# Performance work log

Measured on AMD Instinct MI355X. Metric: run time of the kernel, lower is better.

Reference implementation:

```python
import jax, jax.numpy as jnp
import numpy as np

WL, FL = 64, 40
SCALE = 2.0 ** FL
CLIP_MAX = 2.0 ** (WL - FL - 1) - 2.0 ** (-FL)  # (2^(wl-1)-1)/2^fl
CLIP_MIN = -(2.0 ** (WL - FL - 1))
EPS = 1e-5
H = 8  # num_heads


def quant(x):
    # Fixed-point nearest-rounding quantizer: wl=64, fl=40.
    return jnp.clip(jnp.round(x * SCALE) / SCALE, CLIP_MIN, CLIP_MAX)


def setup_inputs() -> dict:
    key = jax.random.key(0)
    ks = jax.random.split(key, 9)
    N, S, C = 4096, 31, 512  # S = num_particles + 1 = 31 (hard-coded in module)
    SS = S * S
    return {
        "x": jax.random.normal(ks[0], (N, S, C), dtype=jnp.float32),
        "norm_gamma": jnp.ones((C,), jnp.float32),
        "norm_beta": jnp.zeros((C,), jnp.float32),
        "wq": jax.random.normal(ks[1], (C, C), jnp.float32) * 0.02,
        "wk": jax.random.normal(ks[2], (C, C), jnp.float32) * 0.02,
        "wv": jax.random.normal(ks[3], (C, C), jnp.float32) * 0.02,
        "wo": jax.random.normal(ks[4], (C, C), jnp.float32) * 0.02,
        "bo": jnp.zeros((C,), jnp.float32),
        "pre_gamma": jnp.ones((SS,), jnp.float32),
        "pre_beta": jnp.zeros((SS,), jnp.float32),
    }


def reference(x, norm_gamma, norm_beta, wq, wk, wv, wo, bo, pre_gamma, pre_beta):
    N, S, C = x.shape
    # BatchNorm1d(C) on x.transpose(1,2): per-channel stats over (batch, seq), training-mode (batch stats)
    mu = jnp.mean(x, axis=(0, 1))
    var = jnp.var(x, axis=(0, 1))
    out = quant((x - mu) * jax.lax.rsqrt(var + EPS) * norm_gamma + norm_beta)

    out_q = quant(out @ wq.T)
    out_k = quant(out @ wk.T)
    out_v = quant(out @ wv.T)

    q_ = out_q.reshape(N, S, H, C // H)
    k_ = out_k.reshape(N, S, H, C // H)
    v_ = out_v.reshape(N, S, H, C // H)

    energy = quant(jnp.einsum('nqhc,nkhc->nhqk', q_, k_))  # [N,H,S,S]

    # pre_exp_norm: BatchNorm1d(S*S) over reshaped energies; channel dim = S*S, stats over (batch, heads)
    e = energy.reshape(N, H, S * S)
    em = jnp.mean(e, axis=(0, 1))
    ev = jnp.var(e, axis=(0, 1))
    en = quant((e - em) * jax.lax.rsqrt(ev + EPS) * pre_gamma + pre_beta)
    energy_post = en.reshape(N, H, S, S)

    attention = quant(jax.nn.softmax(energy_post / jnp.sqrt(jnp.float32(C)), axis=-1))

    out = quant(jnp.einsum('nhql,nlhc->nqhc', attention, v_)).reshape(N, S, C)
    out = quant(out @ wo.T + bo)
    return quant(out + x)
```

## Files before the change

### kernel.cpp

```cpp
#include <hip/hip_runtime.h>
#include <cstdint>
#include <cstddef>

#define N_ 4096
#define S_ 31
#define C_ 512
#define H_ 8
#define M_ (N_*S_)
#define NH_ (N_*H_)

typedef unsigned short u16;
typedef unsigned char  u8;
typedef __bf16 v8bf __attribute__((ext_vector_type(8)));
typedef float  v4f  __attribute__((ext_vector_type(4)));
typedef float  v2f  __attribute__((ext_vector_type(2)));
typedef unsigned short v8u __attribute__((ext_vector_type(8)));
typedef unsigned short v4u __attribute__((ext_vector_type(4)));

#define WS_STATS 2097152
#define WS_Q (WS_STATS + 32768)
#define WS_K (WS_Q + 67108864)
#define WS_V (WS_K + 67108864)

#define SCALE_QK 16.0f
#define SCALE_V  16.0f

__device__ __forceinline__ u16 f2bf(float f) {
  union { float f; unsigned u; } v; v.f = f;
  unsigned r = v.u + 0x7FFFu + ((v.u >> 16) & 1u);
  return (u16)(r >> 16);
}
__device__ __forceinline__ float bf2f(u16 v) {
  union { unsigned u; float f; } w; w.u = ((unsigned)v) << 16; return w.f;
}
__device__ __forceinline__ unsigned enc4(float a, float b, float c, float d) {
  int w = __builtin_amdgcn_cvt_pk_fp8_f32(a, b, 0, false);
  w = __builtin_amdgcn_cvt_pk_fp8_f32(c, d, w, true);
  return (unsigned)w;
}
__device__ __forceinline__ v8bf dec8(uint2 u) {
  v2f p0 = __builtin_amdgcn_cvt_pk_f32_fp8((int)u.x, false);
  v2f p1 = __builtin_amdgcn_cvt_pk_f32_fp8((int)u.x, true);
  v2f p2 = __builtin_amdgcn_cvt_pk_f32_fp8((int)u.y, false);
  v2f p3 = __builtin_amdgcn_cvt_pk_f32_fp8((int)u.y, true);
  v8bf r;
  r[0]=(__bf16)p0[0]; r[1]=(__bf16)p0[1]; r[2]=(__bf16)p1[0]; r[3]=(__bf16)p1[1];
  r[4]=(__bf16)p2[0]; r[5]=(__bf16)p2[1]; r[6]=(__bf16)p3[0]; r[7]=(__bf16)p3[1];
  return r;
}

__global__ void k_init(const float* wq, const float* wk, const float* wv, const float* wo,
                       u16* wbf, float* statsf) {
  int gid = blockIdx.x * 256 + threadIdx.x;
  if (gid < 6144) statsf[gid] = 0.0f;
  int m = gid >> 18, o = gid & 262143;
  int e    = o & 7;
  int lane = (o >> 3) & 63;
  int kk   = (o >> 9) & 15;
  int j16  = o >> 13;
  int j = j16 * 16 + (lane & 15);
  int k = kk * 32 + (lane >> 4) * 8 + e;
  const float* src = (m == 0) ? wq : (m == 1) ? wk : (m == 2) ? wv : wo;
  wbf[(size_t)m * 262144 + o] = f2bf(src[j * 512 + k]);
}

__global__ void __launch_bounds__(512, 8) k_xstats(const float* __restrict__ x, float* statsf) {
  __shared__ float4 rs[512], rq[512];
  int t = threadIdx.x;
  int c4 = (t & 127) * 4;
  int r0 = blockIdx.x * 128 + (t >> 7) * 32;
  float4 s = {0,0,0,0}, sq = {0,0,0,0};
  const float* p = x + (size_t)r0 * C_ + c4;
  for (int i = 0; i < 32; ++i) {
    float4 v = *(const float4*)(p + (size_t)i * C_);
    s.x += v.x; s.y += v.y; s.z += v.z; s.w += v.w;
    sq.x += v.x*v.x; sq.y += v.y*v.y; sq.z += v.z*v.z; sq.w += v.w*v.w;
  }
  rs[t] = s; rq[t] = sq;
  __syncthreads();
  if (t < 128) {
    #pragma unroll
    for (int g = 1; g < 4; ++g) {
      float4 a = rs[t + g*128], b = rq[t + g*128];
      s.x += a.x; s.y += a.y; s.z += a.z; s.w += a.w;
      sq.x += b.x; sq.y += b.y; sq.z += b.z; sq.w += b.w;
    }
    atomicAdd(&statsf[c4+0], s.x); atomicAdd(&statsf[c4+1], s.y);
    atomicAdd(&statsf[c4+2], s.z); atomicAdd(&statsf[c4+3], s.w);
    atomicAdd(&statsf[512+c4+0], sq.x); atomicAdd(&statsf[512+c4+1], sq.y);
    atomicAdd(&statsf[512+c4+2], sq.z); atomicAdd(&statsf[512+c4+3], sq.w);
  }
}

__device__ __forceinline__ void gemm64(const u16* sa, const u16* B0, v4f (&acc)[4][4], int lane) {
  #pragma unroll
  for (int m = 0; m < 4; ++m)
    #pragma unroll
    for (int c = 0; c < 4; ++c) acc[m][c] = (v4f){0,0,0,0};
  #pragma unroll 2
  for (int kk = 0; kk < 16; ++kk) {
    v8bf a[4], b[4];
    #pragma unroll
    for (int m = 0; m < 4; ++m)
      a[m] = *(const v8bf*)(sa + ((((kk*4 + m) << 6) | (lane ^ (kk & 7))) << 3));
    #pragma unroll
    for (int c = 0; c < 4; ++c)
      b[c] = *(const v8bf*)(B0 + (size_t)c * 8192 + kk * 512);
    #pragma unroll
    for (int m = 0; m < 4; ++m)
      #pragma unroll
      for (int c = 0; c < 4; ++c)
        acc[m][c] = __builtin_amdgcn_mfma_f32_16x16x32_bf16(a[m], b[c], acc[m][c], 0, 0, 0);
  }
}

__global__ void __launch_bounds__(512, 4)
k_qkv(const float* __restrict__ x, const u16* __restrict__ wbf,
      const float* __restrict__ statsf, const float* __restrict__ gamma,
      const float* __restrict__ beta, u8* __restrict__ eg8, u8* __restrict__ vt) {
  __shared__ float s_scale[C_], s_shift[C_];
  __shared__ u16 s_a[16*4*64*8];
  int t = threadIdx.x, nblk = blockIdx.x;
  int wave = t >> 6, lane = t & 63, l15 = lane & 15, quad = lane >> 4;
  {
    float su = statsf[t], sqv = statsf[512 + t];
    float mu  = su * (1.0f / (float)M_);
    float var = sqv * (1.0f / (float)M_) - mu * mu;
    float sc  = rsqrtf(var + 1e-5f) * gamma[t];
    s_scale[t] = sc;
    s_shift[t] = beta[t] - mu * sc;
  }
  __syncthreads();

  const float* xb = x + (size_t)nblk * 2 * S_ * C_;
  for (int it = 0; it < 8; ++it) {
    int idx = t + it * 512;
    int row = idx >> 6, c8 = (idx & 63) << 3;
    int nl = row >> 5, s = row & 31;
    int kk = c8 >> 5, q4 = (c8 >> 3) & 3, mt = row >> 4, r15 = row & 15;
    u16* dst = s_a + ((((kk*4 + mt) << 6) | ((q4*16 + r15) ^ (kk & 7))) << 3);
    v8u o;
    if (s == 31) { o = (v8u){0,0,0,0,0,0,0,0}; }
    else {
      const float* g = xb + (size_t)(nl * 31 + s) * C_ + c8;
      float4 a = *(const float4*)g, b = *(const float4*)(g + 4);
      o[0]=f2bf(a.x*s_scale[c8+0]+s_shift[c8+0]); o[1]=f2bf(a.y*s_scale[c8+1]+s_shift[c8+1]);
      o[2]=f2bf(a.z*s_scale[c8+2]+s_shift[c8+2]); o[3]=f2bf(a.w*s_scale[c8+3]+s_shift[c8+3]);
      o[4]=f2bf(b.x*s_scale[c8+4]+s_shift[c8+4]); o[5]=f2bf(b.y*s_scale[c8+5]+s_shift[c8+5]);
      o[6]=f2bf(b.z*s_scale[c8+6]+s_shift[c8+6]); o[7]=f2bf(b.w*s_scale[c8+7]+s_shift[c8+7]);
    }
    *(v8u*)dst = o;
  }
  __syncthreads();

  v4f acc[4][4];

  gemm64(s_a, wbf + (size_t)2 * 262144 + (size_t)wave * 32768 + (size_t)lane * 8, acc, lane);
  #pragma unroll
  for (int m = 0; m < 4; ++m) {
    int rbase = m*16 + quad*4;
    int nl = rbase >> 5, s0 = rbase & 31;
    size_t nbase = (size_t)(nblk*2 + nl) * 8;
    #pragma unroll
    for (int c = 0; c < 4; ++c) {
      int d = c*16 + l15;
      unsigned w = enc4(acc[m][c][0]*SCALE_V, acc[m][c][1]*SCALE_V,
                        acc[m][c][2]*SCALE_V, acc[m][c][3]*SCALE_V);
      *(unsigned*)(vt + ((nbase + wave) * 2048) + d*32 + s0) = w;
    }
  }

  unsigned qpack[16];
  gemm64(s_a, wbf + (size_t)0 * 262144 + (size_t)wave * 32768 + (size_t)lane * 8, acc, lane);
  #pragma unroll
  for (int m = 0; m < 4; ++m)
    #pragma unroll
    for (int c = 0; c < 4; ++c)
      qpack[m*4+c] = enc4(acc[m][c][0]*SCALE_QK, acc[m][c][1]*SCALE_QK,
                          acc[m][c][2]*SCALE_QK, acc[m][c][3]*SCALE_QK);

  unsigned kpack[16];
  gemm64(s_a, wbf + (size_t)1 * 262144 + (size_t)wave * 32768 + (size_t)lane * 8, acc, lane);
  #pragma unroll
  for (int m = 0; m < 4; ++m)
    #pragma unroll
    for (int c = 0; c < 4; ++c)
      kpack[m*4+c] = enc4(acc[m][c][0]*SCALE_QK, acc[m][c][1]*SCALE_QK,
                          acc[m][c][2]*SCALE_QK, acc[m][c][3]*SCALE_QK);

  __syncthreads();

  u8* scr = (u8*)s_a + wave * 8192;
  #pragma unroll
  for (int m = 0; m < 4; ++m)
    #pragma unroll
    for (int c = 0; c < 4; ++c) {
      int d = c*16 + l15;
      #pragma unroll
      for (int reg = 0; reg < 4; ++reg) {
        int r = m*16 + quad*4 + reg;
        int dd = d ^ ((r & 7) << 3);
        scr[r*64 + dd]        = (u8)(qpack[m*4+c] >> (reg*8));
        scr[4096 + r*64 + dd] = (u8)(kpack[m*4+c] >> (reg*8));
      }
    }

  const float inv = 1.0f / (SCALE_QK * SCALE_QK);
  #pragma unroll 1
  for (int n = 0; n < 2; ++n) {
    v8bf A[2][2], B[2][2];
    #pragma unroll
    for (int mt = 0; mt < 2; ++mt)
      #pragma unroll
      for (int kk = 0; kk < 2; ++kk) {
        int r = n*32 + mt*16 + l15;
        int dA = (kk*32 + quad*8) ^ ((r & 7) << 3);
        A[mt][kk] = dec8(*(const uint2*)(scr + r*64 + dA));
        B[mt][kk] = dec8(*(const uint2*)(scr + 4096 + r*64 + dA));
      }
    u16* ep = (u16*)(eg8 + (((size_t)(nblk*2 + n) * 8 + wave) * 2048));
    #pragma unroll
    for (int qt = 0; qt < 2; ++qt)
      #pragma unroll
      for (int kt = 0; kt < 2; ++kt) {
        v4f a2 = {0,0,0,0};
        a2 = __builtin_amdgcn_mfma_f32_16x16x32_bf16(A[qt][0], B[kt][0], a2, 0, 0, 0);
        a2 = __builtin_amdgcn_mfma_f32_16x16x32_bf16(A[qt][1], B[kt][1], a2, 0, 0, 0);
        int k = kt*16 + l15;
        #pragma unroll
        for (int reg = 0; reg < 4; ++reg) {
          int q = qt*16 + quad*4 + reg;
          ep[q*32 + k] = f2bf(a2[reg] * inv);
        }
      }
  }
}

__global__ void __launch_bounds__(256, 8) k_estats(const u16* __restrict__ eg, float* statsf) {
  int t = threadIdx.x;
  int r0 = blockIdx.x * 32;
  float s[4] = {0,0,0,0}, sq[4] = {0,0,0,0};
  for (int i = 0; i < 32; ++i) {
    uint2 u = *(const uint2*)(eg + (size_t)(r0 + i) * 1024 + t * 4);
    float v0 = bf2f((u16)(u.x & 0xffff)), v1 = bf2f((u16)(u.x >> 16));
    float v2 = bf2f((u16)(u.y & 0xffff)), v3 = bf2f((u16)(u.y >> 16));
    s[0]+=v0; s[1]+=v1; s[2]+=v2; s[3]+=v3;
    sq[0]+=v0*v0; sq[1]+=v1*v1; sq[2]+=v2*v2; sq[3]+=v3*v3;
  }
  #pragma unroll
  for (int j = 0; j < 4; ++j) {
    atomicAdd(&statsf[2048 + t*4 + j], s[j]);
    atomicAdd(&statsf[3072 + t*4 + j], sq[j]);
  }
}

__global__ void k_finalize_e(const float* pg, const float* pb, float* statsf) {
  int c = threadIdx.x;
  int q = c >> 5, k = c & 31;
  const float invC = 0.04419417382415922f;
  float s2 = 0.f, sh2 = 0.f;
  if (q < 31 && k < 31) {
    int ss = q*31 + k;
    float mu  = statsf[2048 + c] * (1.0f / (float)NH_);
    float var = statsf[3072 + c] * (1.0f / (float)NH_) - mu * mu;
    float sc  = rsqrtf(var + 1e-5f) * pg[ss];
    s2  = sc * invC;
    sh2 = (pb[ss] - mu * sc) * invC;
  }
  statsf[4096 + c] = s2;
  statsf[5120 + c] = sh2;
}

__global__ void __launch_bounds__(512, 4)
k_oproj(const float* __restrict__ x, const u16* __restrict__ wbf,
        const float* __restrict__ statsf, const u16* __restrict__ eg,
        const u8* __restrict__ vt, const float* __restrict__ bo, float* __restrict__ out) {
  __shared__ u16 s_a[16*4*64*8];
  __shared__ u16 s_attn[8][1024];
  int t = threadIdx.x, nblk = blockIdx.x;
  int wave = t >> 6, lane = t & 63, l15 = lane & 15, quad = lane >> 4;

  int q = lane & 31, half = lane >> 5;
  #pragma unroll 1
  for (int tk = 0; tk < 2; ++tk) {
    int task = wave * 2 + tk;
    int nl = task >> 3, h = task & 7;
    size_t nh = (size_t)(nblk*2 + nl) * 8 + h;
    const u16* ep = eg + nh * 1024;
    int cb = q*32 + half*16;
    v8u e0 = *(const v8u*)(ep + cb);
    v8u e1 = *(const v8u*)(ep + cb + 8);
    const float* s2g  = statsf + 4096 + cb;
    const float* sh2g = statsf + 5120 + cb;
    float lg[16];
    #pragma unroll
    for (int j = 0; j < 8; ++j) lg[j]   = bf2f(e0[j]) * s2g[j]   + sh2g[j];
    #pragma unroll
    for (int j = 0; j < 8; ++j) lg[8+j] = bf2f(e1[j]) * s2g[8+j] + sh2g[8+j];
    if (half) lg[15] = -1e30f;
    float mx = lg[0];
    #pragma unroll
    for (int j = 1; j < 16; ++j) mx = fmaxf(mx, lg[j]);
    mx = fmaxf(mx, __shfl_xor(mx, 32));
    float sum = 0.f;
    #pragma unroll
    for (int j = 0; j < 16; ++j) { lg[j] = __expf(lg[j] - mx); sum += lg[j]; }
    sum += __shfl_xor(sum, 32);
    float r = (q == 31) ? 0.f : (1.0f / sum);
    v8u o0, o1;
    #pragma unroll
    for (int j = 0; j < 8; ++j) { o0[j] = f2bf(lg[j] * r); o1[j] = f2bf(lg[8+j] * r); }
    *(v8u*)(&s_attn[wave][cb]) = o0;
    *(v8u*)(&s_attn[wave][cb + 8]) = o1;
    v8bf a0 = *(const v8bf*)(&s_attn[wave][(l15)*32 + quad*8]);
    v8bf a1 = *(const v8bf*)(&s_attn[wave][(16 + l15)*32 + quad*8]);
    const float invV = 1.0f / SCALE_V;
    #pragma unroll
    for (int ct = 0; ct < 4; ++ct) {
      uint2 u = *(const uint2*)(vt + nh*2048 + (ct*16 + l15)*32 + quad*8);
      v8bf b = dec8(u);
      v4f c0 = {0,0,0,0}, c1 = {0,0,0,0};
      c0 = __builtin_amdgcn_mfma_f32_16x16x32_bf16(b, a0, c0, 0, 0, 0);
      c1 = __builtin_amdgcn_mfma_f32_16x16x32_bf16(b, a1, c1, 0, 0, 0);
      int kkA = h*2 + (ct>>1);
      int qA  = (ct*2 + (quad>>1)) & 3;
      int pA  = (quad&1)*4;
      v4u w0, w1;
      #pragma unroll
      for (int reg = 0; reg < 4; ++reg) {
        w0[reg] = f2bf(c0[reg] * invV);
        w1[reg] = f2bf(c1[reg] * invV);
      }
      *(v4u*)(&s_a[((((kkA*4 + nl*2 + 0) << 6) | (qA*16 + l15)) << 3) + pA]) = w0;
      *(v4u*)(&s_a[((((kkA*4 + nl*2 + 1) << 6) | (qA*16 + l15)) << 3) + pA]) = w1;
    }
  }
  __syncthreads();

  {
    const u16* B0 = wbf + (size_t)3 * 262144 + (size_t)wave * 32768 + (size_t)lane * 8;
    v4f acc[4][4];
    #pragma unroll
    for (int m = 0; m < 4; ++m)
      #pragma unroll
      for (int c = 0; c < 4; ++c) acc[m][c] = (v4f){0,0,0,0};
    #pragma unroll 2
    for (int kk = 0; kk < 16; ++kk) {
      v8bf a[4], b[4];
      #pragma unroll
      for (int m = 0; m < 4; ++m)
        a[m] = *(const v8bf*)(s_a + ((((kk*4 + m) << 6) | lane) << 3));
      #pragma unroll
      for (int c = 0; c < 4; ++c)
        b[c] = *(const v8bf*)(B0 + (size_t)c * 8192 + kk * 512);
      #pragma unroll
      for (int m = 0; m < 4; ++m)
        #pragma unroll
        for (int c = 0; c < 4; ++c)
          acc[m][c] = __builtin_amdgcn_mfma_f32_16x16x32_bf16(a[m], b[c], acc[m][c], 0, 0, 0);
    }
    #pragma unroll
    for (int m = 0; m < 4; ++m) {
      int rbase = m*16 + quad*4;
      int nl = rbase >> 5, s0 = rbase & 31;
      #pragma unroll
      for (int c = 0; c < 4; ++c) {
        int j = wave*64 + c*16 + l15;
        float bj = bo[j];
        #pragma unroll
        for (int reg = 0; reg < 4; ++reg) {
          int s = s0 + reg;
          if (s < 31) {
            size_t off = (size_t)((nblk*2 + nl) * 31 + s) * C_ + j;
            out[off] = acc[m][c][reg] + bj + x[off];
          }
        }
      }
    }
  }
}

extern "C" void kernel_launch(void* const* d_in, const int* in_sizes, int n_in,
                              void* d_out, int out_size, void* d_ws, size_t ws_size,
                              hipStream_t stream) {
  const float* x     = (const float*)d_in[0];
  const float* gamma = (const float*)d_in[1];
  const float* beta  = (const float*)d_in[2];
  const float* wq    = (const float*)d_in[3];
  const float* wk    = (const float*)d_in[4];
  const float* wv    = (const float*)d_in[5];
  const float* wo    = (const float*)d_in[6];
  const float* bo    = (const float*)d_in[7];
  const float* pg    = (const float*)d_in[8];
  const float* pb    = (const float*)d_in[9];

  char* ws = (char*)d_ws;
  u16*   wbf    = (u16*)ws;
  float* statsf = (float*)(ws + WS_STATS);
  u8*    eg8    = (u8*)(ws + WS_Q);
  u8*    vtp    = (u8*)(ws + WS_V);
  float* outp   = (float*)d_out;

  k_init<<<4096, 256, 0, stream>>>(wq, wk, wv, wo, wbf, statsf);
  k_xstats<<<992, 512, 0, stream>>>(x, statsf);
  k_qkv<<<2048, 512, 0, stream>>>(x, wbf, statsf, gamma, beta, eg8, vtp);
  k_estats<<<1024, 256, 0, stream>>>((const u16*)eg8, statsf);
  k_finalize_e<<<1, 1024, 0, stream>>>(pg, pb, statsf);
  k_oproj<<<2048, 512, 0, stream>>>(x, wbf, statsf, (const u16*)eg8, vtp, bo, outp);
}
```

Measured before the change: 1.009 ms.

## Split GEMM tiles into 64x32 halves with register-prefetched weight fragments

Each wave's 64x64 GEMM tile is now computed as two 64x32 halves, so it holds 8 accumulators instead of 16. A three-slot rotating buffer prefetches the global weight fragments two k-steps ahead, hiding global load latency behind the MFMAs. The intent is to cut register pressure to fit the launch bound of 4 blocks per CU and to overlap weight loads with compute. In exchange, the LDS A fragments are read twice per tile, and the fully unrolled loop grows code size.

```diff
diff --git a/kernel.cpp b/kernel.cpp
--- a/kernel.cpp
+++ b/kernel.cpp
@@ -92,25 +92,34 @@
   }
 }
 
-__device__ __forceinline__ void gemm64(const u16* sa, const u16* B0, v4f (&acc)[4][4], int lane) {
+template<int SWZ>
+__device__ __forceinline__ void gemm64x32(const u16* sa, const u16* B0, v4f (&acc)[4][2], int lane) {
   #pragma unroll
   for (int m = 0; m < 4; ++m)
     #pragma unroll
-    for (int c = 0; c < 4; ++c) acc[m][c] = (v4f){0,0,0,0};
-  #pragma unroll 2
+    for (int c = 0; c < 2; ++c) acc[m][c] = (v4f){0,0,0,0};
+  v8bf b[3][2];
+  #pragma unroll
+  for (int p = 0; p < 2; ++p)
+    #pragma unroll
+    for (int c = 0; c < 2; ++c)
+      b[p][c] = *(const v8bf*)(B0 + (size_t)c * 8192 + p * 512);
+  #pragma unroll
   for (int kk = 0; kk < 16; ++kk) {
-    v8bf a[4], b[4];
+    if (kk + 2 < 16) {
+      #pragma unroll
+      for (int c = 0; c < 2; ++c)
+        b[(kk+2)%3][c] = *(const v8bf*)(B0 + (size_t)c * 8192 + (kk+2) * 512);
+    }
+    v8bf a[4];
     #pragma unroll
     for (int m = 0; m < 4; ++m)
-      a[m] = *(const v8bf*)(sa + ((((kk*4 + m) << 6) | (lane ^ (kk & 7))) << 3));
-    #pragma unroll
-    for (int c = 0; c < 4; ++c)
-      b[c] = *(const v8bf*)(B0 + (size_t)c * 8192 + kk * 512);
+      a[m] = *(const v8bf*)(sa + ((((kk*4 + m) << 6) | (SWZ ? (lane ^ (kk & 7)) : lane)) << 3));
     #pragma unroll
     for (int m = 0; m < 4; ++m)
       #pragma unroll
-      for (int c = 0; c < 4; ++c)
-        acc[m][c] = __builtin_amdgcn_mfma_f32_16x16x32_bf16(a[m], b[c], acc[m][c], 0, 0, 0);
+      for (int c = 0; c < 2; ++c)
+        acc[m][c] = __builtin_amdgcn_mfma_f32_16x16x32_bf16(a[m], b[kk%3][c], acc[m][c], 0, 0, 0);
   }
 }
 
@@ -153,40 +162,50 @@
   }
   __syncthreads();
 
-  v4f acc[4][4];
-
-  gemm64(s_a, wbf + (size_t)2 * 262144 + (size_t)wave * 32768 + (size_t)lane * 8, acc, lane);
-  #pragma unroll
-  for (int m = 0; m < 4; ++m) {
-    int rbase = m*16 + quad*4;
-    int nl = rbase >> 5, s0 = rbase & 31;
-    size_t nbase = (size_t)(nblk*2 + nl) * 8;
-    #pragma unroll
-    for (int c = 0; c < 4; ++c) {
-      int d = c*16 + l15;
-      unsigned w = enc4(acc[m][c][0]*SCALE_V, acc[m][c][1]*SCALE_V,
-                        acc[m][c][2]*SCALE_V, acc[m][c][3]*SCALE_V);
-      *(unsigned*)(vt + ((nbase + wave) * 2048) + d*32 + s0) = w;
+  #pragma unroll
+  for (int cs = 0; cs < 2; ++cs) {
+    v4f acc[4][2];
+    gemm64x32<1>(s_a, wbf + (size_t)2 * 262144 + (size_t)wave * 32768 + cs * 16384 + (size_t)lane * 8, acc, lane);
+    #pragma unroll
+    for (int m = 0; m < 4; ++m) {
+      int rbase = m*16 + quad*4;
+      int nl = rbase >> 5, s0 = rbase & 31;
+      size_t nbase = (size_t)(nblk*2 + nl) * 8;
+      #pragma unroll
+      for (int c = 0; c < 2; ++c) {
+        int d = cs*32 + c*16 + l15;
+        unsigned w = enc4(acc[m][c][0]*SCALE_V, acc[m][c][1]*SCALE_V,
+                          acc[m][c][2]*SCALE_V, acc[m][c][3]*SCALE_V);
+        *(unsigned*)(vt + ((nbase + wave) * 2048) + d*32 + s0) = w;
+      }
     }
   }
 
   unsigned qpack[16];
-  gemm64(s_a, wbf + (size_t)0 * 262144 + (size_t)wave * 32768 + (size_t)lane * 8, acc, lane);
-  #pragma unroll
-  for (int m = 0; m < 4; ++m)
-    #pragma unroll
-    for (int c = 0; c < 4; ++c)
-      qpack[m*4+c] = enc4(acc[m][c][0]*SCALE_QK, acc[m][c][1]*SCALE_QK,
-                          acc[m][c][2]*SCALE_QK, acc[m][c][3]*SCALE_QK);
+  #pragma unroll
+  for (int cs = 0; cs < 2; ++cs) {
+    v4f acc[4][2];
+    gemm64x32<1>(s_a, wbf + (size_t)0 * 262144 + (size_t)wave * 32768 + cs * 16384 + (size_t)lane * 8, acc, lane);
+    #pragma unroll
+    for (int m = 0; m < 4; ++m)
+      #pragma unroll
+      for (int c = 0; c < 2; ++c)
+        qpack[m*4 + cs*2 + c] = enc4(acc[m][c][0]*SCALE_QK, acc[m][c][1]*SCALE_QK,
+                                     acc[m][c][2]*SCALE_QK, acc[m][c][3]*SCALE_QK);
+  }
 
   unsigned kpack[16];
-  gemm64(s_a, wbf + (size_t)1 * 262144 + (size_t)wave * 32768 + (size_t)lane * 8, acc, lane);
-  #pragma unroll
-  for (int m = 0; m < 4; ++m)
-    #pragma unroll
-    for (int c = 0; c < 4; ++c)
-      kpack[m*4+c] = enc4(acc[m][c][0]*SCALE_QK, acc[m][c][1]*SCALE_QK,
-                          acc[m][c][2]*SCALE_QK, acc[m][c][3]*SCALE_QK);
+  #pragma unroll
+  for (int cs = 0; cs < 2; ++cs) {
+    v4f acc[4][2];
+    gemm64x32<1>(s_a, wbf + (size_t)1 * 262144 + (size_t)wave * 32768 + cs * 16384 + (size_t)lane * 8, acc, lane);
+    #pragma unroll
+    for (int m = 0; m < 4; ++m)
+      #pragma unroll
+      for (int c = 0; c < 2; ++c)
+        kpack[m*4 + cs*2 + c] = enc4(acc[m][c][0]*SCALE_QK, acc[m][c][1]*SCALE_QK,
+                                     acc[m][c][2]*SCALE_QK, acc[m][c][3]*SCALE_QK);
+  }
 
   __syncthreads();
 
@@ -337,35 +356,17 @@
   }
   __syncthreads();
 
-  {
-    const u16* B0 = wbf + (size_t)3 * 262144 + (size_t)wave * 32768 + (size_t)lane * 8;
-    v4f acc[4][4];
-    #pragma unroll
-    for (int m = 0; m < 4; ++m)
-      #pragma unroll
-      for (int c = 0; c < 4; ++c) acc[m][c] = (v4f){0,0,0,0};
-    #pragma unroll 2
-    for (int kk = 0; kk < 16; ++kk) {
-      v8bf a[4], b[4];
-      #pragma unroll
-      for (int m = 0; m < 4; ++m)
-        a[m] = *(const v8bf*)(s_a + ((((kk*4 + m) << 6) | lane) << 3));
-      #pragma unroll
-      for (int c = 0; c < 4; ++c)
-        b[c] = *(const v8bf*)(B0 + (size_t)c * 8192 + kk * 512);
-      #pragma unroll
-      for (int m = 0; m < 4; ++m)
-        #pragma unroll
-        for (int c = 0; c < 4; ++c)
-          acc[m][c] = __builtin_amdgcn_mfma_f32_16x16x32_bf16(a[m], b[c], acc[m][c], 0, 0, 0);
-    }
+  #pragma unroll
+  for (int cs = 0; cs < 2; ++cs) {
+    v4f acc[4][2];
+    gemm64x32<0>(s_a, wbf + (size_t)3 * 262144 + (size_t)wave * 32768 + cs * 16384 + (size_t)lane * 8, acc, lane);
     #pragma unroll
     for (int m = 0; m < 4; ++m) {
       int rbase = m*16 + quad*4;
       int nl = rbase >> 5, s0 = rbase & 31;
       #pragma unroll
-      for (int c = 0; c < 4; ++c) {
-        int j = wave*64 + c*16 + l15;
+      for (int c = 0; c < 2; ++c) {
+        int j = wave*64 + cs*32 + c*16 + l15;
         float bj = bo[j];
         #pragma unroll
         for (int reg = 0; reg < 4; ++reg) {
```

Result: slower. 2.620 ms (+159.5%).
